# Kernel tuning notes

Hardware: AMD Instinct MI355X
Metric: run time of the kernel (lower is better)

The kernel has to match this reference:

```python
import jax, jax.numpy as jnp
import numpy as np
from jax.ops import segment_sum

N, E, D, H = 50000, 800000, 128, 128


def setup_inputs() -> dict:
    key = jax.random.key(0)
    ks = jax.random.split(key, 8)
    x = jax.random.normal(ks[0], (N, D), dtype=jnp.float32)
    edge_index = jax.random.randint(ks[1], (2, E), 0, N, dtype=jnp.int64)
    # Glorot-ish scaled weights for 3 GCNConv layers
    s0 = 1.0 / np.sqrt(D)
    s1 = 1.0 / np.sqrt(H)
    W0 = jax.random.normal(ks[2], (D, H), dtype=jnp.float32) * s0
    W1 = jax.random.normal(ks[3], (H, H), dtype=jnp.float32) * s1
    W2 = jax.random.normal(ks[4], (H, H), dtype=jnp.float32) * s1
    b0 = jnp.zeros((H,), dtype=jnp.float32)
    b1 = jnp.zeros((H,), dtype=jnp.float32)
    b2 = jnp.zeros((H,), dtype=jnp.float32)
    return {"x": x, "edge_index": edge_index,
            "W0": W0, "b0": b0, "W1": W1, "b1": b1, "W2": W2, "b2": b2}


def _gcn_norm(edge_index, num_nodes):
    # Add self-loops, compute symmetric normalization deg^-1/2 A deg^-1/2
    loops = jnp.arange(num_nodes, dtype=edge_index.dtype)
    src = jnp.concatenate([edge_index[0], loops])  # [E+N]
    dst = jnp.concatenate([edge_index[1], loops])  # [E+N]
    deg = segment_sum(jnp.ones_like(dst, dtype=jnp.float32), dst,
                      num_segments=num_nodes)       # in-degree incl. self-loop
    dinv = jnp.where(deg > 0, jax.lax.rsqrt(deg), 0.0)
    norm = dinv[src] * dinv[dst]                    # [E+N]
    return src, dst, norm


def _gcn_conv(x, src, dst, norm, W, b, num_nodes):
    h = x @ W                                        # [N, H] linear first (PyG order)
    msg = h[src] * norm[:, None]                     # gather + scale
    agg = segment_sum(msg, dst, num_segments=num_nodes)  # scatter-add
    return agg + b


def reference(x, edge_index, W0, b0, W1, b1, W2, b2):
    num_nodes = x.shape[0]
    src, dst, norm = _gcn_norm(edge_index, num_nodes)
    for W, b in ((W0, b0), (W1, b1), (W2, b2)):
        x = jax.nn.relu(_gcn_conv(x, src, dst, norm, W, b, num_nodes))
    return x
```

## Files before the change

### kernel.cpp

```cpp
#include <hip/hip_runtime.h>


typedef __attribute__((ext_vector_type(8))) unsigned short ushort8;
typedef __attribute__((ext_vector_type(8))) short short8v;
typedef __attribute__((ext_vector_type(4))) float f32x4;

__device__ __forceinline__ unsigned short f2bf(float f) {
    unsigned u = __float_as_uint(f);
    unsigned r = (u + 0x7FFF + ((u >> 16) & 1)) >> 16;
    return (unsigned short)r;
}
__device__ __forceinline__ float bf2f(unsigned short s) {
    return __uint_as_float(((unsigned)s) << 16);
}

__global__ __launch_bounds__(256) void zero_kernel(int4* __restrict__ p, int n4) {
    int i = blockIdx.x * 256 + threadIdx.x;
    if (i < n4) p[i] = make_int4(0, 0, 0, 0);
}

__global__ void count_rank_kernel(const int* __restrict__ ei, int* __restrict__ cnt,
                                  int* __restrict__ rank, int E) {
    int e = blockIdx.x * blockDim.x + threadIdx.x;
    if (e < E) rank[e] = atomicAdd(&cnt[ei[E + e]], 1);
}

__global__ __launch_bounds__(256) void block_sum_kernel(const int* __restrict__ cnt,
                                                        int* __restrict__ bsum, int n) {
    int i = blockIdx.x * 256 + threadIdx.x;
    int v = (i < n) ? cnt[i] : 0;
#pragma unroll
    for (int off = 32; off; off >>= 1) v += __shfl_down(v, off);
    __shared__ int ws[4];
    int lane = threadIdx.x & 63, w = threadIdx.x >> 6;
    if (lane == 0) ws[w] = v;
    __syncthreads();
    if (threadIdx.x == 0) bsum[blockIdx.x] = ws[0] + ws[1] + ws[2] + ws[3];
}

__global__ __launch_bounds__(256) void scan_partials_kernel(const int* __restrict__ bsum,
                                                            int* __restrict__ bpre,
                                                            int* __restrict__ rowptr,
                                                            int nb, int n) {
    __shared__ int sh[256];
    int t = threadIdx.x;
    int v = (t < nb) ? bsum[t] : 0;
    sh[t] = v;
    __syncthreads();
    for (int off = 1; off < 256; off <<= 1) {
        int u = (t >= off) ? sh[t - off] : 0;
        __syncthreads();
        sh[t] += u;
        __syncthreads();
    }
    if (t < nb) bpre[t] = sh[t] - v;
    if (t == 255) rowptr[n] = sh[255];
}

__global__ __launch_bounds__(256) void scan_write_kernel(const int* __restrict__ cnt,
                                                         const int* __restrict__ bpre,
                                                         int* __restrict__ rowptr,
                                                         float* __restrict__ dinv, int n) {
    __shared__ int sh[256];
    int t = threadIdx.x;
    int i = blockIdx.x * 256 + t;
    int c = (i < n) ? cnt[i] : 0;
    sh[t] = c;
    __syncthreads();
    for (int off = 1; off < 256; off <<= 1) {
        int u = (t >= off) ? sh[t - off] : 0;
        __syncthreads();
        sh[t] += u;
        __syncthreads();
    }
    if (i < n) {
        rowptr[i] = bpre[blockIdx.x] + sh[t] - c;
        dinv[i] = rsqrtf((float)(c + 1));
    }
}

__global__ void fill_kernel(const int* __restrict__ ei, const int* __restrict__ rowptr,
                            const int* __restrict__ rank, int* __restrict__ col, int E) {
    int e = blockIdx.x * blockDim.x + threadIdx.x;
    if (e < E) {
        int d = ei[E + e];
        col[rowptr[d] + rank[e]] = ei[e];
    }
}

__global__ __launch_bounds__(256) void wprep_kernel(const float* __restrict__ W,
                                                    short* __restrict__ Wfrag) {
    int idx = blockIdx.x * 256 + threadIdx.x;
    int l = idx & 63;
    int cks = idx >> 6;
    int ks = cks & 3, c = cks >> 2;
    int col = c * 16 + (l & 15);
    int k0 = ks * 32 + (l >> 4) * 8;
    short8v o;
#pragma unroll
    for (int j = 0; j < 8; ++j) o[j] = (short)f2bf(W[(size_t)(k0 + j) * 128 + col]);
    ((short8v*)Wfrag)[idx] = o;
}

__global__ __launch_bounds__(256) void gemm_mfma_kernel(const float* __restrict__ X,
                                                        const short* __restrict__ Wfrag,
                                                        const float* __restrict__ dinv,
                                                        unsigned short* __restrict__ G, int n) {
    int t = threadIdx.x;
    int wv = t >> 6, l = t & 63;
    int row0 = blockIdx.x * 64 + wv * 16;
    int r = l & 15, half = l >> 4;
    int arow = row0 + r;
    bool rok = arow < n;

    f32x4 acc[8];
#pragma unroll
    for (int c = 0; c < 8; ++c) acc[c] = (f32x4){0.f, 0.f, 0.f, 0.f};

    const short8v* WF = (const short8v*)Wfrag;

#pragma unroll
    for (int ks = 0; ks < 4; ++ks) {
        short8v a = (short8v){0, 0, 0, 0, 0, 0, 0, 0};
        if (rok) {
            const float4* xp = (const float4*)(X + (size_t)arow * 128 + ks * 32 + half * 8);
            float4 x0 = xp[0], x1 = xp[1];
            a[0] = (short)f2bf(x0.x); a[1] = (short)f2bf(x0.y);
            a[2] = (short)f2bf(x0.z); a[3] = (short)f2bf(x0.w);
            a[4] = (short)f2bf(x1.x); a[5] = (short)f2bf(x1.y);
            a[6] = (short)f2bf(x1.z); a[7] = (short)f2bf(x1.w);
        }
#pragma unroll
        for (int c = 0; c < 8; ++c) {
            short8v b = WF[(c * 4 + ks) * 64 + l];
            acc[c] = __builtin_amdgcn_mfma_f32_16x16x32_bf16(a, b, acc[c], 0, 0, 0);
        }
    }

    float ds[4];
    int orow[4];
#pragma unroll
    for (int i = 0; i < 4; ++i) {
        orow[i] = row0 + half * 4 + i;
        ds[i] = (orow[i] < n) ? dinv[orow[i]] : 0.f;
    }
#pragma unroll
    for (int c = 0; c < 8; ++c) {
#pragma unroll
        for (int i = 0; i < 4; ++i) {
            if (orow[i] < n)
                G[(size_t)orow[i] * 128 + c * 16 + r] = f2bf(ds[i] * acc[c][i]);
        }
    }
}

__global__ __launch_bounds__(256) void agg_kernel(const unsigned short* __restrict__ G,
                                                  const int* __restrict__ rowptr,
                                                  const int* __restrict__ col,
                                                  const float* __restrict__ dinv,
                                                  const float* __restrict__ b,
                                                  float* __restrict__ out, int n) {
    int gw = (int)((blockIdx.x * blockDim.x + threadIdx.x) >> 6);
    if (gw >= n) return;
    int lane = threadIdx.x & 63;
    int q = lane & 15, p = lane >> 4;
    int beg = rowptr[gw], end = rowptr[gw + 1];
    float di = dinv[gw];

    float acc[8];
#pragma unroll
    for (int j = 0; j < 8; ++j) acc[j] = 0.f;

    int e = beg;
    for (; e + 16 <= end; e += 16) {
        int c0 = col[e + p];
        int c1 = col[e + 4 + p];
        int c2 = col[e + 8 + p];
        int c3 = col[e + 12 + p];
        ushort8 h0 = *(const ushort8*)(G + (size_t)c0 * 128 + q * 8);
        ushort8 h1 = *(const ushort8*)(G + (size_t)c1 * 128 + q * 8);
        ushort8 h2 = *(const ushort8*)(G + (size_t)c2 * 128 + q * 8);
        ushort8 h3 = *(const ushort8*)(G + (size_t)c3 * 128 + q * 8);
#pragma unroll
        for (int j = 0; j < 8; ++j)
            acc[j] += (bf2f(h0[j]) + bf2f(h1[j])) + (bf2f(h2[j]) + bf2f(h3[j]));
    }
    for (; e + 4 <= end; e += 4) {
        int c0 = col[e + p];
        ushort8 h0 = *(const ushort8*)(G + (size_t)c0 * 128 + q * 8);
#pragma unroll
        for (int j = 0; j < 8; ++j) acc[j] += bf2f(h0[j]);
    }
    if (e < end) {
        int idx = e + p;
        bool valid = idx < end;
        int c0 = col[valid ? idx : e];
        float w = valid ? 1.f : 0.f;
        ushort8 h0 = *(const ushort8*)(G + (size_t)c0 * 128 + q * 8);
#pragma unroll
        for (int j = 0; j < 8; ++j) acc[j] = fmaf(w, bf2f(h0[j]), acc[j]);
    }
#pragma unroll
    for (int j = 0; j < 8; ++j) {
        acc[j] += __shfl_xor(acc[j], 16);
        acc[j] += __shfl_xor(acc[j], 32);
    }

    if (p == 0) {
        ushort8 gs = *(const ushort8*)(G + (size_t)gw * 128 + q * 8);
        float4 b0 = *(const float4*)(b + q * 8);
        float4 b1 = *(const float4*)(b + q * 8 + 4);
        float o[8];
#pragma unroll
        for (int j = 0; j < 8; ++j) o[j] = di * (acc[j] + bf2f(gs[j]));
        o[0] += b0.x; o[1] += b0.y; o[2] += b0.z; o[3] += b0.w;
        o[4] += b1.x; o[5] += b1.y; o[6] += b1.z; o[7] += b1.w;
        float4 w0 = make_float4(fmaxf(o[0], 0.f), fmaxf(o[1], 0.f), fmaxf(o[2], 0.f), fmaxf(o[3], 0.f));
        float4 w1 = make_float4(fmaxf(o[4], 0.f), fmaxf(o[5], 0.f), fmaxf(o[6], 0.f), fmaxf(o[7], 0.f));
        *(float4*)(out + (size_t)gw * 128 + q * 8)     = w0;
        *(float4*)(out + (size_t)gw * 128 + q * 8 + 4) = w1;
    }
}

extern "C" void kernel_launch(void* const* d_in, const int* in_sizes, int n_in,
                              void* d_out, int out_size, void* d_ws, size_t ws_size,
                              hipStream_t stream) {
    const float* x  = (const float*)d_in[0];
    const int*   ei = (const int*)d_in[1];
    const float* W0 = (const float*)d_in[2];
    const float* b0 = (const float*)d_in[3];
    const float* W1 = (const float*)d_in[4];
    const float* b1 = (const float*)d_in[5];
    const float* W2 = (const float*)d_in[6];
    const float* b2 = (const float*)d_in[7];
    float* out = (float*)d_out;

    int N = in_sizes[0] / 128;
    int E = in_sizes[1] / 2;
    int nb = (N + 255) / 256;

    char* wsb = (char*)d_ws;
    size_t off = 0;
    auto alloc = [&](size_t bytes) -> void* {
        void* p = wsb + off;
        off = (off + bytes + 255) & ~(size_t)255;
        return p;
    };
    int*   cnt    = (int*)  alloc((size_t)N * 4);
    int*   rowptr = (int*)  alloc((size_t)(N + 1) * 4);
    float* dinv   = (float*)alloc((size_t)N * 4);
    int*   bsum   = (int*)  alloc((size_t)nb * 4);
    int*   bpre   = (int*)  alloc((size_t)nb * 4);
    int*   rank   = (int*)  alloc((size_t)E * 4);
    int*   col    = (int*)  alloc((size_t)E * 4);
    unsigned short* g = (unsigned short*)alloc((size_t)N * 128 * 2);
    float* xA     = (float*)alloc((size_t)N * 128 * 4);
    short* wf0    = (short*)alloc(128 * 128 * 2);
    short* wf1    = (short*)alloc(128 * 128 * 2);
    short* wf2    = (short*)alloc(128 * 128 * 2);

    int n4 = (N + 3) / 4;
    zero_kernel<<<(n4 + 255) / 256, 256, 0, stream>>>((int4*)cnt, n4);
    count_rank_kernel<<<(E + 255) / 256, 256, 0, stream>>>(ei, cnt, rank, E);
    block_sum_kernel<<<nb, 256, 0, stream>>>(cnt, bsum, N);
    scan_partials_kernel<<<1, 256, 0, stream>>>(bsum, bpre, rowptr, nb, N);
    scan_write_kernel<<<nb, 256, 0, stream>>>(cnt, bpre, rowptr, dinv, N);
    fill_kernel<<<(E + 255) / 256, 256, 0, stream>>>(ei, rowptr, rank, col, E);
    wprep_kernel<<<8, 256, 0, stream>>>(W0, wf0);
    wprep_kernel<<<8, 256, 0, stream>>>(W1, wf1);
    wprep_kernel<<<8, 256, 0, stream>>>(W2, wf2);

    int gblk = (N + 63) / 64;
    int ablk = (N + 3) / 4;

    gemm_mfma_kernel<<<gblk, 256, 0, stream>>>(x,  wf0, dinv, g, N);
    agg_kernel<<<ablk, 256, 0, stream>>>(g, rowptr, col, dinv, b0, xA, N);

    gemm_mfma_kernel<<<gblk, 256, 0, stream>>>(xA, wf1, dinv, g, N);
    agg_kernel<<<ablk, 256, 0, stream>>>(g, rowptr, col, dinv, b1, xA, N);

    gemm_mfma_kernel<<<gblk, 256, 0, stream>>>(xA, wf2, dinv, g, N);
    agg_kernel<<<ablk, 256, 0, stream>>>(g, rowptr, col, dinv, b2, out, N);
}
```

Measured before the change: 218.5 us.

## Store intermediate activations in bf16, software-pipeline aggregation gathers, merge weight prep

The aggregation kernel now writes the intermediate layer activations as bf16, and the GEMM reads those bf16 rows directly. This halves the activation write and read traffic between layers. The aggregation gather loop is rewritten as a double-buffered, masked prefetch over 8 edges per step, and the self-row load is hoisted to the top of the kernel. The three weight-prep launches are merged into one. The bf16 rounding happens at the same point the GEMM already rounded to bf16, so accuracy should barely change. The predicated loop wastes some loads on low-degree nodes.

```diff
diff --git a/kernel.cpp b/kernel.cpp
--- a/kernel.cpp
+++ b/kernel.cpp
@@ -88,9 +88,16 @@
     }
 }
 
-__global__ __launch_bounds__(256) void wprep_kernel(const float* __restrict__ W,
-                                                    short* __restrict__ Wfrag) {
-    int idx = blockIdx.x * 256 + threadIdx.x;
+__global__ __launch_bounds__(256) void wprep_kernel(const float* __restrict__ W0,
+                                                    const float* __restrict__ W1,
+                                                    const float* __restrict__ W2,
+                                                    short* __restrict__ F0,
+                                                    short* __restrict__ F1,
+                                                    short* __restrict__ F2) {
+    int which = blockIdx.x >> 3;
+    const float* W = which == 0 ? W0 : (which == 1 ? W1 : W2);
+    short* Wfrag   = which == 0 ? F0 : (which == 1 ? F1 : F2);
+    int idx = (blockIdx.x & 7) * 256 + threadIdx.x;
     int l = idx & 63;
     int cks = idx >> 6;
     int ks = cks & 3, c = cks >> 2;
@@ -102,7 +109,8 @@
     ((short8v*)Wfrag)[idx] = o;
 }
 
-__global__ __launch_bounds__(256) void gemm_mfma_kernel(const float* __restrict__ X,
+template <bool IN_BF16>
+__global__ __launch_bounds__(256) void gemm_mfma_kernel(const void* __restrict__ Xv,
                                                         const short* __restrict__ Wfrag,
                                                         const float* __restrict__ dinv,
                                                         unsigned short* __restrict__ G, int n) {
@@ -123,12 +131,18 @@
     for (int ks = 0; ks < 4; ++ks) {
         short8v a = (short8v){0, 0, 0, 0, 0, 0, 0, 0};
         if (rok) {
-            const float4* xp = (const float4*)(X + (size_t)arow * 128 + ks * 32 + half * 8);
-            float4 x0 = xp[0], x1 = xp[1];
-            a[0] = (short)f2bf(x0.x); a[1] = (short)f2bf(x0.y);
-            a[2] = (short)f2bf(x0.z); a[3] = (short)f2bf(x0.w);
-            a[4] = (short)f2bf(x1.x); a[5] = (short)f2bf(x1.y);
-            a[6] = (short)f2bf(x1.z); a[7] = (short)f2bf(x1.w);
+            if (IN_BF16) {
+                const unsigned short* X = (const unsigned short*)Xv;
+                a = *(const short8v*)(X + (size_t)arow * 128 + ks * 32 + half * 8);
+            } else {
+                const float* X = (const float*)Xv;
+                const float4* xp = (const float4*)(X + (size_t)arow * 128 + ks * 32 + half * 8);
+                float4 x0 = xp[0], x1 = xp[1];
+                a[0] = (short)f2bf(x0.x); a[1] = (short)f2bf(x0.y);
+                a[2] = (short)f2bf(x0.z); a[3] = (short)f2bf(x0.w);
+                a[4] = (short)f2bf(x1.x); a[5] = (short)f2bf(x1.y);
+                a[6] = (short)f2bf(x1.z); a[7] = (short)f2bf(x1.w);
+            }
         }
 #pragma unroll
         for (int c = 0; c < 8; ++c) {
@@ -154,12 +168,13 @@
     }
 }
 
+template <bool OUT_BF16>
 __global__ __launch_bounds__(256) void agg_kernel(const unsigned short* __restrict__ G,
                                                   const int* __restrict__ rowptr,
                                                   const int* __restrict__ col,
                                                   const float* __restrict__ dinv,
                                                   const float* __restrict__ b,
-                                                  float* __restrict__ out, int n) {
+                                                  void* __restrict__ outv, int n) {
     int gw = (int)((blockIdx.x * blockDim.x + threadIdx.x) >> 6);
     if (gw >= n) return;
     int lane = threadIdx.x & 63;
@@ -167,39 +182,42 @@
     int beg = rowptr[gw], end = rowptr[gw + 1];
     float di = dinv[gw];
 
+    ushort8 gs = *(const ushort8*)(G + (size_t)gw * 128 + q * 8);
+
     float acc[8];
 #pragma unroll
     for (int j = 0; j < 8; ++j) acc[j] = 0.f;
 
-    int e = beg;
-    for (; e + 16 <= end; e += 16) {
-        int c0 = col[e + p];
-        int c1 = col[e + 4 + p];
-        int c2 = col[e + 8 + p];
-        int c3 = col[e + 12 + p];
-        ushort8 h0 = *(const ushort8*)(G + (size_t)c0 * 128 + q * 8);
-        ushort8 h1 = *(const ushort8*)(G + (size_t)c1 * 128 + q * 8);
-        ushort8 h2 = *(const ushort8*)(G + (size_t)c2 * 128 + q * 8);
-        ushort8 h3 = *(const ushort8*)(G + (size_t)c3 * 128 + q * 8);
-#pragma unroll
-        for (int j = 0; j < 8; ++j)
-            acc[j] += (bf2f(h0[j]) + bf2f(h1[j])) + (bf2f(h2[j]) + bf2f(h3[j]));
-    }
-    for (; e + 4 <= end; e += 4) {
-        int c0 = col[e + p];
-        ushort8 h0 = *(const ushort8*)(G + (size_t)c0 * 128 + q * 8);
-#pragma unroll
-        for (int j = 0; j < 8; ++j) acc[j] += bf2f(h0[j]);
-    }
-    if (e < end) {
-        int idx = e + p;
-        bool valid = idx < end;
-        int c0 = col[valid ? idx : e];
-        float w = valid ? 1.f : 0.f;
-        ushort8 h0 = *(const ushort8*)(G + (size_t)c0 * 128 + q * 8);
-#pragma unroll
-        for (int j = 0; j < 8; ++j) acc[j] = fmaf(w, bf2f(h0[j]), acc[j]);
-    }
+    int deg = end - beg;
+    int nit = (deg + 7) >> 3;
+
+    ushort8 h0a, h1a, h0b, h1b;
+    float m0a = 0.f, m1a = 0.f, m0b = 0.f, m1b = 0.f;
+
+    auto issue = [&](int s, ushort8& h0, ushort8& h1, float& m0, float& m1) {
+        int i0 = beg + s * 8 + p;
+        int i1 = i0 + 4;
+        bool v0 = i0 < end, v1 = i1 < end;
+        int c0 = col[v0 ? i0 : 0];
+        int c1 = col[v1 ? i1 : 0];
+        m0 = v0 ? 1.f : 0.f;
+        m1 = v1 ? 1.f : 0.f;
+        h0 = *(const ushort8*)(G + (size_t)c0 * 128 + q * 8);
+        h1 = *(const ushort8*)(G + (size_t)c1 * 128 + q * 8);
+    };
+
+    if (nit > 0) issue(0, h0a, h1a, m0a, m1a);
+    if (nit > 1) issue(1, h0b, h1b, m0b, m1b);
+    for (int s = 0; s < nit; ++s) {
+#pragma unroll
+        for (int j = 0; j < 8; ++j) {
+            acc[j] = fmaf(m0a, bf2f(h0a[j]), acc[j]);
+            acc[j] = fmaf(m1a, bf2f(h1a[j]), acc[j]);
+        }
+        h0a = h0b; h1a = h1b; m0a = m0b; m1a = m1b;
+        if (s + 2 < nit) issue(s + 2, h0b, h1b, m0b, m1b);
+    }
+
 #pragma unroll
     for (int j = 0; j < 8; ++j) {
         acc[j] += __shfl_xor(acc[j], 16);
@@ -207,7 +225,6 @@
     }
 
     if (p == 0) {
-        ushort8 gs = *(const ushort8*)(G + (size_t)gw * 128 + q * 8);
         float4 b0 = *(const float4*)(b + q * 8);
         float4 b1 = *(const float4*)(b + q * 8 + 4);
         float o[8];
@@ -215,10 +232,18 @@
         for (int j = 0; j < 8; ++j) o[j] = di * (acc[j] + bf2f(gs[j]));
         o[0] += b0.x; o[1] += b0.y; o[2] += b0.z; o[3] += b0.w;
         o[4] += b1.x; o[5] += b1.y; o[6] += b1.z; o[7] += b1.w;
-        float4 w0 = make_float4(fmaxf(o[0], 0.f), fmaxf(o[1], 0.f), fmaxf(o[2], 0.f), fmaxf(o[3], 0.f));
-        float4 w1 = make_float4(fmaxf(o[4], 0.f), fmaxf(o[5], 0.f), fmaxf(o[6], 0.f), fmaxf(o[7], 0.f));
-        *(float4*)(out + (size_t)gw * 128 + q * 8)     = w0;
-        *(float4*)(out + (size_t)gw * 128 + q * 8 + 4) = w1;
+#pragma unroll
+        for (int j = 0; j < 8; ++j) o[j] = fmaxf(o[j], 0.f);
+        if (OUT_BF16) {
+            ushort8 ov;
+#pragma unroll
+            for (int j = 0; j < 8; ++j) ov[j] = f2bf(o[j]);
+            *(ushort8*)((unsigned short*)outv + (size_t)gw * 128 + q * 8) = ov;
+        } else {
+            float* out = (float*)outv;
+            *(float4*)(out + (size_t)gw * 128 + q * 8)     = make_float4(o[0], o[1], o[2], o[3]);
+            *(float4*)(out + (size_t)gw * 128 + q * 8 + 4) = make_float4(o[4], o[5], o[6], o[7]);
+        }
     }
 }
 
@@ -253,8 +278,8 @@
     int*   bpre   = (int*)  alloc((size_t)nb * 4);
     int*   rank   = (int*)  alloc((size_t)E * 4);
     int*   col    = (int*)  alloc((size_t)E * 4);
-    unsigned short* g = (unsigned short*)alloc((size_t)N * 128 * 2);
-    float* xA     = (float*)alloc((size_t)N * 128 * 4);
+    unsigned short* g  = (unsigned short*)alloc((size_t)N * 128 * 2);
+    unsigned short* xB = (unsigned short*)alloc((size_t)N * 128 * 2);
     short* wf0    = (short*)alloc(128 * 128 * 2);
     short* wf1    = (short*)alloc(128 * 128 * 2);
     short* wf2    = (short*)alloc(128 * 128 * 2);
@@ -266,19 +291,17 @@
     scan_partials_kernel<<<1, 256, 0, stream>>>(bsum, bpre, rowptr, nb, N);
     scan_write_kernel<<<nb, 256, 0, stream>>>(cnt, bpre, rowptr, dinv, N);
     fill_kernel<<<(E + 255) / 256, 256, 0, stream>>>(ei, rowptr, rank, col, E);
-    wprep_kernel<<<8, 256, 0, stream>>>(W0, wf0);
-    wprep_kernel<<<8, 256, 0, stream>>>(W1, wf1);
-    wprep_kernel<<<8, 256, 0, stream>>>(W2, wf2);
+    wprep_kernel<<<24, 256, 0, stream>>>(W0, W1, W2, wf0, wf1, wf2);
 
     int gblk = (N + 63) / 64;
     int ablk = (N + 3) / 4;
 
-    gemm_mfma_kernel<<<gblk, 256, 0, stream>>>(x,  wf0, dinv, g, N);
-    agg_kernel<<<ablk, 256, 0, stream>>>(g, rowptr, col, dinv, b0, xA, N);
-
-    gemm_mfma_kernel<<<gblk, 256, 0, stream>>>(xA, wf1, dinv, g, N);
-    agg_kernel<<<ablk, 256, 0, stream>>>(g, rowptr, col, dinv, b1, xA, N);
-
-    gemm_mfma_kernel<<<gblk, 256, 0, stream>>>(xA, wf2, dinv, g, N);
-    agg_kernel<<<ablk, 256, 0, stream>>>(g, rowptr, col, dinv, b2, out, N);
-}
+    gemm_mfma_kernel<false><<<gblk, 256, 0, stream>>>(x,  wf0, dinv, g, N);
+    agg_kernel<true><<<ablk, 256, 0, stream>>>(g, rowptr, col, dinv, b0, xB, N);
+
+    gemm_mfma_kernel<true><<<gblk, 256, 0, stream>>>(xB, wf1, dinv, g, N);
+    agg_kernel<true><<<ablk, 256, 0, stream>>>(g, rowptr, col, dinv, b1, xB, N);
+
+    gemm_mfma_kernel<true><<<gblk, 256, 0, stream>>>(xB, wf2, dinv, g, N);
+    agg_kernel<false><<<ablk, 256, 0, stream>>>(g, rowptr, col, dinv, b2, out, N);
+}
```

After: 214.0 us. -2.0%, faster.
